# Kernel optimization log

Measured on AMD Instinct MI355X. Metric: run time of the kernel, lower is better.

## Reference

```python
import jax, jax.numpy as jnp
import numpy as np

DIM = 1024
NUM_HEADS = 16
HEAD_DIM = DIM // NUM_HEADS


def setup_inputs() -> dict:
    key = jax.random.key(0)
    ks = jax.random.split(key, 6)
    B, N, C = 2, 2048, DIM
    s = 1.0 / np.sqrt(C)
    return {
        "x": jax.random.normal(ks[0], (B, N, C), dtype=jnp.float32),
        "Wq": jax.random.normal(ks[1], (C, C), dtype=jnp.float32) * s,
        "Wk": jax.random.normal(ks[2], (C, C), dtype=jnp.float32) * s,
        "Wv": jax.random.normal(ks[3], (C, C), dtype=jnp.float32) * s,
        "Wproj": jax.random.normal(ks[4], (C, C), dtype=jnp.float32) * s,
        "bproj": jax.random.normal(ks[5], (C,), dtype=jnp.float32) * 0.01,
    }


def reference(x, Wq, Wk, Wv, Wproj, bproj):
    B, N, C = x.shape
    H, D = NUM_HEADS, HEAD_DIM
    scale = D ** -0.5
    # Linear (torch convention: y = x @ W.T), then split heads -> [B, H, N, D]
    q = (x @ Wq.T).reshape(B, N, H, D).transpose(0, 2, 1, 3)
    k = (x @ Wk.T).reshape(B, N, H, D).transpose(0, 2, 1, 3)
    v = (x @ Wv.T).reshape(B, N, H, D).transpose(0, 2, 1, 3)
    attn = jnp.einsum("bhnd,bhmd->bhnm", q, k) * scale  # [B,H,N,N]
    attn = jax.nn.softmax(attn, axis=-1)
    out = jnp.einsum("bhnm,bhmd->bhnd", attn, v)  # [B,H,N,D]
    out = out.transpose(0, 2, 1, 3).reshape(B, N, C)
    return out @ Wproj.T + bproj
```

## Files before the change

kernel.cpp:

```cpp
#include <hip/hip_runtime.h>
#include <stdint.h>

typedef unsigned short u16;
typedef unsigned int u32;

typedef __bf16 bf16x8 __attribute__((ext_vector_type(8)));
typedef float f32x4 __attribute__((ext_vector_type(4)));

#define LOG2E_SCALE 0.18033688011112042f

static __device__ __forceinline__ u16 f2bf(float f) {
  union { float f; u32 u; } v; v.f = f;
  u32 r = v.u + 0x7fffu + ((v.u >> 16) & 1u);
  return (u16)(r >> 16);
}
static __device__ __forceinline__ u32 pk2(float a, float b) {
  u32 r;
  asm("v_cvt_pk_bf16_f32 %0, %1, %2" : "=v"(r) : "v"(a), "v"(b));
  return r;
}
static __device__ __forceinline__ float fexp2(float x) {
  return __builtin_amdgcn_exp2f(x);
}
static __device__ __forceinline__ float blo(u32 u) {
  union { u32 u; float f; } v; v.u = u << 16; return v.f;
}
static __device__ __forceinline__ float bhi(u32 u) {
  union { u32 u; float f; } v; v.u = u & 0xffff0000u; return v.f;
}

static __device__ __forceinline__ void gl_lds16(const void* g, void* l) {
  __builtin_amdgcn_global_load_lds(
      (const __attribute__((address_space(1))) u32*)g,
      (__attribute__((address_space(3))) u32*)l, 16, 0, 0);
}

__global__ void cast_kernel(const float* __restrict__ x, const float* __restrict__ wq,
                            const float* __restrict__ wk, const float* __restrict__ wv,
                            const float* __restrict__ wp,
                            u16* __restrict__ xb, u16* __restrict__ wqb, u16* __restrict__ wkb,
                            u16* __restrict__ wvb, u16* __restrict__ wpb) {
  const float* src; u16* dst; int n;
  switch (blockIdx.y) {
    case 0: src = x;  dst = xb;  n = 4194304; break;
    case 1: src = wq; dst = wqb; n = 1048576; break;
    case 2: src = wk; dst = wkb; n = 1048576; break;
    case 3: src = wv; dst = wvb; n = 1048576; break;
    default: src = wp; dst = wpb; n = 1048576; break;
  }
  int i = (blockIdx.x * 256 + threadIdx.x) * 8;
  if (i >= n) return;
  float4 a = *(const float4*)(src + i);
  float4 b = *(const float4*)(src + i + 4);
  uint4 o;
  o.x = pk2(a.x, a.y); o.y = pk2(a.z, a.w);
  o.z = pk2(b.x, b.y); o.w = pk2(b.z, b.w);
  *(uint4*)(dst + i) = o;
}

__global__ __launch_bounds__(256, 3) void gemm_qkv(
    const u16* __restrict__ A, const u16* __restrict__ Bq, const u16* __restrict__ Bk,
    const u16* __restrict__ Bv, u16* __restrict__ oQ, u16* __restrict__ oK,
    u16* __restrict__ oVt)
{
  constexpr int K = 1024;
  __shared__ u16 As[128 * 32];
  __shared__ u16 Bs[128 * 32];
  __shared__ float tbuf[4][16 * 68];

  const int tid  = threadIdx.x;
  const int lane = tid & 63;
  const int wave = tid >> 6;
  const int cl   = lane & 15;
  const int g    = lane >> 4;
  const int wm   = (wave >> 1) * 64;
  const int wn   = (wave & 1) * 64;
  const int bm   = blockIdx.y * 128;
  const int bn   = blockIdx.x * 128;
  const int z    = blockIdx.z;
  const u16* B = (z == 0 ? Bq : (z == 1 ? Bk : Bv));

  f32x4 zero4 = {0.f, 0.f, 0.f, 0.f};
  f32x4 acc[4][4];
#pragma unroll
  for (int i = 0; i < 4; i++)
#pragma unroll
    for (int j = 0; j < 4; j++) acc[i][j] = zero4;

  const int srow = tid >> 2;
  const int sch  = (tid & 3) ^ ((srow >> 1) & 3);
  const char* aG = (const char*)(A + (size_t)(bm + srow) * K) + sch * 16;
  const char* bG = (const char*)(B + (size_t)(bn + srow) * K) + sch * 16;
  char* aL = (char*)As + tid * 16;
  char* bL = (char*)Bs + tid * 16;
  const size_t rstep = (size_t)64 * K * 2;

  const int swz = (cl >> 1) & 3;

  for (int k0 = 0; k0 < K; k0 += 32) {
    gl_lds16(aG + k0 * 2, aL);
    gl_lds16(aG + rstep + k0 * 2, aL + 4096);
    gl_lds16(bG + k0 * 2, bL);
    gl_lds16(bG + rstep + k0 * 2, bL + 4096);
    __syncthreads();

    bf16x8 af[4], bf[4];
#pragma unroll
    for (int i = 0; i < 4; i++)
      af[i] = *(const bf16x8*)(As + (wm + i * 16 + cl) * 32 + ((g ^ swz) & 3) * 8);
#pragma unroll
    for (int j = 0; j < 4; j++)
      bf[j] = *(const bf16x8*)(Bs + (wn + j * 16 + cl) * 32 + ((g ^ swz) & 3) * 8);
#pragma unroll
    for (int i = 0; i < 4; i++)
#pragma unroll
      for (int j = 0; j < 4; j++)
        acc[i][j] = __builtin_amdgcn_mfma_f32_16x16x32_bf16(af[i], bf[j], acc[i][j], 0, 0, 0);
    __syncthreads();
  }

  const int rq = g * 4;
  if (z <= 1) {
    u16* o = z ? oK : oQ;
    const float cs = z ? 1.0f : LOG2E_SCALE;
#pragma unroll
    for (int i = 0; i < 4; i++)
#pragma unroll
      for (int j = 0; j < 4; j++)
#pragma unroll
        for (int r = 0; r < 4; r++) {
          int gm = bm + wm + i * 16 + rq + r;
          int gn = bn + wn + j * 16 + cl;
          int b = gm >> 11, ns = gm & 2047;
          int h = gn >> 6,  d  = gn & 63;
          o[(((size_t)(b * 16 + h)) * 2048 + ns) * 64 + d] = f2bf(acc[i][j][r] * cs);
        }
  } else {
    float* tb = tbuf[wave];
#pragma unroll
    for (int j = 0; j < 4; j++) {
      asm volatile("s_waitcnt lgkmcnt(0)" ::: "memory");
#pragma unroll
      for (int i = 0; i < 4; i++)
        *(f32x4*)(tb + cl * 68 + i * 16 + rq) = acc[i][j];
      asm volatile("s_waitcnt lgkmcnt(0)" ::: "memory");
#pragma unroll
      for (int half = 0; half < 2; half++) {
        int dd = lane >> 2, p = (lane & 3) + half * 4;
        f32x4 x0 = *(const f32x4*)(tb + dd * 68 + p * 8);
        f32x4 x1 = *(const f32x4*)(tb + dd * 68 + p * 8 + 4);
        uint4 pkd;
        pkd.x = pk2(x0[0], x0[1]); pkd.y = pk2(x0[2], x0[3]);
        pkd.z = pk2(x1[0], x1[1]); pkd.w = pk2(x1[2], x1[3]);
        int gn = bn + wn + j * 16 + dd;
        int gm = bm + wm + p * 8;
        int b = gm >> 11, nn = gm & 2047;
        int h = gn >> 6,  dl = gn & 63;
        *(uint4*)(oVt + (((size_t)(b * 16 + h)) * 64 + dl) * 2048 + nn) = pkd;
      }
    }
  }
}

__global__ __launch_bounds__(512, 6) void attn_kernel(
    const u16* __restrict__ Q, const u16* __restrict__ Km,
    const u16* __restrict__ Vt, u16* __restrict__ Op, float* __restrict__ lp)
{
  __shared__ u16 ks[2][64 * 64];
  __shared__ u16 vs[2][64 * 64];
  __shared__ u16 ps[128 * 36];

  const int tid  = threadIdx.x;
  const int lane = tid & 63;
  const int W    = tid >> 6;
  const int cl   = lane & 15;
  const int g    = lane >> 4;
  const int bh   = blockIdx.x;
  const int qt   = blockIdx.y;
  const int sp   = blockIdx.z;

  const char* kS = (const char*)Km + (size_t)bh * 2048 * 128 + (size_t)sp * 1024 * 128;
  const char* vS = (const char*)Vt + (size_t)bh * 64 * 4096 + (size_t)sp * 2048;

  const u16* qbase = Q + ((size_t)bh * 2048 + qt * 128 + W * 16) * 64;
  bf16x8 qf[2];
#pragma unroll
  for (int h = 0; h < 2; h++)
    qf[h] = *(const bf16x8*)(qbase + cl * 64 + h * 32 + g * 8);

  auto stage_k = [&](int t) {
    const char* kT = kS + (size_t)t * 8192;
    int kv = tid >> 3, s = tid & 7;
    gl_lds16(kT + kv * 128 + (((s ^ kv) & 7) * 16), (char*)ks[t & 1] + tid * 16);
  };
  auto stage_v = [&](int t) {
    const char* vT = vS + (size_t)t * 128;
    int d = tid >> 3, s = tid & 7;
    gl_lds16(vT + (size_t)d * 4096 + (((s ^ d) & 7) * 16), (char*)vs[t & 1] + tid * 16);
  };

  stage_k(0);
  stage_v(0);

  f32x4 zero4 = {0.f, 0.f, 0.f, 0.f};
  f32x4 o_acc[4];
#pragma unroll
  for (int j = 0; j < 4; j++) o_acc[j] = zero4;
  float li = 0.f;

  for (int t = 0; t < 16; ++t) {
    __syncthreads();
    if (t < 15) { stage_k(t + 1); stage_v(t + 1); }

    const u16* kb = ks[t & 1];
    const u16* vb = vs[t & 1];

    f32x4 st[4];
#pragma unroll
    for (int j = 0; j < 4; j++) st[j] = zero4;
#pragma unroll
    for (int h = 0; h < 2; h++) {
#pragma unroll
      for (int j = 0; j < 4; j++) {
        bf16x8 kf = *(const bf16x8*)(kb + (j * 16 + cl) * 64 + (((h * 4 + g) ^ (cl & 7)) & 7) * 8);
        st[j] = __builtin_amdgcn_mfma_f32_16x16x32_bf16(kf, qf[h], st[j], 0, 0, 0);
      }
    }

#pragma unroll
    for (int j = 0; j < 4; j++)
#pragma unroll
      for (int r = 0; r < 4; r++) {
        float p = fexp2(st[j][r]);
        st[j][r] = p;
        li += p;
      }

    char* prow = (char*)ps + (W * 16 + cl) * 72;
#pragma unroll
    for (int h32 = 0; h32 < 2; h32++) {
#pragma unroll
      for (int jj = 0; jj < 2; jj++) {
        int j = h32 * 2 + jj;
        uint2 w;
        w.x = pk2(st[j][0], st[j][1]);
        w.y = pk2(st[j][2], st[j][3]);
        *(uint2*)(prow + jj * 32 + g * 8) = w;
      }
      bf16x8 pf, vf[4];
      union { bf16x8 v; uint2 u[2]; } pu;
      pu.u[0] = *(const uint2*)(prow + g * 16);
      pu.u[1] = *(const uint2*)(prow + g * 16 + 8);
      pf = pu.v;
#pragma unroll
      for (int j = 0; j < 4; j++)
        vf[j] = *(const bf16x8*)(vb + (j * 16 + cl) * 64 + (((h32 * 4 + g) ^ (cl & 7)) & 7) * 8);
#pragma unroll
      for (int j = 0; j < 4; j++)
        o_acc[j] = __builtin_amdgcn_mfma_f32_16x16x32_bf16(pf, vf[j], o_acc[j], 0, 0, 0);
    }
  }

  li += __shfl_xor(li, 16, 64);
  li += __shfl_xor(li, 32, 64);
  const int b = bh >> 4, hh = bh & 15;
  u16* Os = Op + (size_t)sp * 4194304;
  float* ls = lp + sp * 65536;
  if (g == 0) ls[bh * 2048 + qt * 128 + W * 16 + cl] = li;
#pragma unroll
  for (int r = 0; r < 4; r++) {
    int row = qt * 128 + W * 16 + g * 4 + r;
    u16* orow = Os + ((size_t)b * 2048 + row) * 1024 + hh * 64;
#pragma unroll
    for (int j = 0; j < 4; j++)
      orow[j * 16 + cl] = f2bf(o_acc[j][r]);
  }
}

__global__ void reduce_o(const u16* __restrict__ Op, const float* __restrict__ lp,
                         u16* __restrict__ Ow) {
  int t = blockIdx.x * 256 + threadIdx.x;
  int idx = t * 8;
  int b   = idx >> 21;
  int rem = idx & 2097151;
  int row = rem >> 10;
  int h   = (rem & 1023) >> 6;
  int lidx = (b * 16 + h) * 2048 + row;
  float inv = 1.0f / (lp[lidx] + lp[65536 + lidx]);
  uint4 a = *(const uint4*)(Op + idx);
  uint4 c = *(const uint4*)(Op + 4194304 + idx);
  uint4 o;
  o.x = pk2((blo(a.x) + blo(c.x)) * inv, (bhi(a.x) + bhi(c.x)) * inv);
  o.y = pk2((blo(a.y) + blo(c.y)) * inv, (bhi(a.y) + bhi(c.y)) * inv);
  o.z = pk2((blo(a.z) + blo(c.z)) * inv, (bhi(a.z) + bhi(c.z)) * inv);
  o.w = pk2((blo(a.w) + blo(c.w)) * inv, (bhi(a.w) + bhi(c.w)) * inv);
  *(uint4*)(Ow + idx) = o;
}

__global__ __launch_bounds__(256, 4) void proj_gemm(
    const u16* __restrict__ A, const u16* __restrict__ B,
    float* __restrict__ out, const float* __restrict__ bias)
{
  constexpr int K = 1024;
  __shared__ u16 As[64 * 32];
  __shared__ u16 Bs[128 * 32];

  const int tid  = threadIdx.x;
  const int lane = tid & 63;
  const int wave = tid >> 6;
  const int cl   = lane & 15;
  const int g    = lane >> 4;
  const int wm   = (wave >> 1) * 32;
  const int wn   = (wave & 1) * 64;
  const int bm   = blockIdx.y * 64;
  const int bn   = blockIdx.x * 128;

  f32x4 zero4 = {0.f, 0.f, 0.f, 0.f};
  f32x4 acc[2][4];
#pragma unroll
  for (int i = 0; i < 2; i++)
#pragma unroll
    for (int j = 0; j < 4; j++) acc[i][j] = zero4;

  const int srow = tid >> 2;
  const int sch  = (tid & 3) ^ ((srow >> 1) & 3);
  const char* aG = (const char*)(A + (size_t)(bm + srow) * K) + sch * 16;
  const char* bG = (const char*)(B + (size_t)(bn + srow) * K) + sch * 16;
  char* aL = (char*)As + tid * 16;
  char* bL = (char*)Bs + tid * 16;
  const size_t rstep = (size_t)64 * K * 2;

  const int swz = (cl >> 1) & 3;

  for (int k0 = 0; k0 < K; k0 += 32) {
    gl_lds16(aG + k0 * 2, aL);
    gl_lds16(bG + k0 * 2, bL);
    gl_lds16(bG + rstep + k0 * 2, bL + 4096);
    __syncthreads();

    bf16x8 af[2], bf[4];
#pragma unroll
    for (int i = 0; i < 2; i++)
      af[i] = *(const bf16x8*)(As + (wm + i * 16 + cl) * 32 + ((g ^ swz) & 3) * 8);
#pragma unroll
    for (int j = 0; j < 4; j++)
      bf[j] = *(const bf16x8*)(Bs + (wn + j * 16 + cl) * 32 + ((g ^ swz) & 3) * 8);
#pragma unroll
    for (int i = 0; i < 2; i++)
#pragma unroll
      for (int j = 0; j < 4; j++)
        acc[i][j] = __builtin_amdgcn_mfma_f32_16x16x32_bf16(af[i], bf[j], acc[i][j], 0, 0, 0);
    __syncthreads();
  }

  const int rq = g * 4;
#pragma unroll
  for (int i = 0; i < 2; i++)
#pragma unroll
    for (int j = 0; j < 4; j++)
#pragma unroll
      for (int r = 0; r < 4; r++) {
        int gm = bm + wm + i * 16 + rq + r;
        int gn = bn + wn + j * 16 + cl;
        out[(size_t)gm * 1024 + gn] = acc[i][j][r] + bias[gn];
      }
}

extern "C" void kernel_launch(void* const* d_in, const int* in_sizes, int n_in,
                              void* d_out, int out_size, void* d_ws, size_t ws_size,
                              hipStream_t stream) {
  const float* x     = (const float*)d_in[0];
  const float* Wq    = (const float*)d_in[1];
  const float* Wk    = (const float*)d_in[2];
  const float* Wv    = (const float*)d_in[3];
  const float* Wp    = (const float*)d_in[4];
  const float* bproj = (const float*)d_in[5];

  u16* ws  = (u16*)d_ws;
  u16* xb  = ws;
  u16* wqb = xb + 4194304;
  u16* wkb = wqb + 1048576;
  u16* wvb = wkb + 1048576;
  u16* wpb = wvb + 1048576;
  u16* Qw  = wpb + 1048576;
  u16* Kw  = Qw + 4194304;
  u16* Vw  = Kw + 4194304;
  u16* Ow  = Vw + 4194304;
  u16* Opart = Ow + 4194304;
  float* lpart = (float*)(Opart + 8388608);
  (void)in_sizes; (void)n_in; (void)out_size; (void)ws_size;

  cast_kernel<<<dim3(2048, 5), 256, 0, stream>>>(x, Wq, Wk, Wv, Wp, xb, wqb, wkb, wvb, wpb);
  gemm_qkv<<<dim3(8, 32, 3), 256, 0, stream>>>(xb, wqb, wkb, wvb, Qw, Kw, Vw);
  attn_kernel<<<dim3(32, 16, 2), 512, 0, stream>>>(Qw, Kw, Vw, Opart, lpart);
  reduce_o<<<dim3(2048), 256, 0, stream>>>(Opart, lpart, Ow);
  proj_gemm<<<dim3(8, 64), 256, 0, stream>>>(Ow, wpb, (float*)d_out, bproj);
}
```

Measured before the change: 183.9 us.

## Double K-tile depth in QKV and projection GEMMs and compute row sums via MFMA

Both GEMM kernels now stage a 64-wide K slab per iteration with an 8-way XOR swizzle, which halves the number of barrier pairs and loop iterations. The QKV kernel reuses the A tile's shared memory as its transpose buffer, so the larger tiles do not increase LDS usage beyond the old footprint. In attention, the softmax denominator is accumulated by an extra MFMA against a ones vector instead of scalar adds and cross-lane shuffles. The cost is one extra MFMA per PV step, and the row sum is now taken over bf16-rounded probabilities rather than fp32 ones.

Result: faster. 178.9 us (-2.7%).

```diff
diff --git a/kernel.cpp b/kernel.cpp
--- a/kernel.cpp
+++ b/kernel.cpp
@@ -64,9 +64,8 @@
     u16* __restrict__ oVt)
 {
   constexpr int K = 1024;
-  __shared__ u16 As[128 * 32];
-  __shared__ u16 Bs[128 * 32];
-  __shared__ float tbuf[4][16 * 68];
+  __shared__ u16 As[128 * 64];
+  __shared__ u16 Bs[128 * 64];
 
   const int tid  = threadIdx.x;
   const int lane = tid & 63;
@@ -87,35 +86,37 @@
 #pragma unroll
     for (int j = 0; j < 4; j++) acc[i][j] = zero4;
 
-  const int srow = tid >> 2;
-  const int sch  = (tid & 3) ^ ((srow >> 1) & 3);
-  const char* aG = (const char*)(A + (size_t)(bm + srow) * K) + sch * 16;
-  const char* bG = (const char*)(B + (size_t)(bn + srow) * K) + sch * 16;
+  const int srow = tid >> 3;
+  const int sch  = (tid & 7) ^ (srow & 7);
+  const char* aG = (const char*)(A + (size_t)(bm + srow) * K + sch * 8);
+  const char* bG = (const char*)(B + (size_t)(bn + srow) * K + sch * 8);
   char* aL = (char*)As + tid * 16;
   char* bL = (char*)Bs + tid * 16;
-  const size_t rstep = (size_t)64 * K * 2;
-
-  const int swz = (cl >> 1) & 3;
-
-  for (int k0 = 0; k0 < K; k0 += 32) {
-    gl_lds16(aG + k0 * 2, aL);
-    gl_lds16(aG + rstep + k0 * 2, aL + 4096);
-    gl_lds16(bG + k0 * 2, bL);
-    gl_lds16(bG + rstep + k0 * 2, bL + 4096);
+  const size_t rstep = (size_t)32 * K * 2;
+
+  for (int k0 = 0; k0 < K; k0 += 64) {
+#pragma unroll
+    for (int r = 0; r < 4; r++) {
+      gl_lds16(aG + r * rstep + k0 * 2, aL + r * 4096);
+      gl_lds16(bG + r * rstep + k0 * 2, bL + r * 4096);
+    }
     __syncthreads();
 
-    bf16x8 af[4], bf[4];
-#pragma unroll
-    for (int i = 0; i < 4; i++)
-      af[i] = *(const bf16x8*)(As + (wm + i * 16 + cl) * 32 + ((g ^ swz) & 3) * 8);
-#pragma unroll
-    for (int j = 0; j < 4; j++)
-      bf[j] = *(const bf16x8*)(Bs + (wn + j * 16 + cl) * 32 + ((g ^ swz) & 3) * 8);
-#pragma unroll
-    for (int i = 0; i < 4; i++)
+#pragma unroll
+    for (int kk = 0; kk < 2; kk++) {
+      bf16x8 af[4], bf[4];
+#pragma unroll
+      for (int i = 0; i < 4; i++)
+        af[i] = *(const bf16x8*)(As + (wm + i * 16 + cl) * 64 + (((kk * 4 + g) ^ (cl & 7)) * 8));
 #pragma unroll
       for (int j = 0; j < 4; j++)
-        acc[i][j] = __builtin_amdgcn_mfma_f32_16x16x32_bf16(af[i], bf[j], acc[i][j], 0, 0, 0);
+        bf[j] = *(const bf16x8*)(Bs + (wn + j * 16 + cl) * 64 + (((kk * 4 + g) ^ (cl & 7)) * 8));
+#pragma unroll
+      for (int i = 0; i < 4; i++)
+#pragma unroll
+        for (int j = 0; j < 4; j++)
+          acc[i][j] = __builtin_amdgcn_mfma_f32_16x16x32_bf16(af[i], bf[j], acc[i][j], 0, 0, 0);
+    }
     __syncthreads();
   }
 
@@ -136,7 +137,7 @@
           o[(((size_t)(b * 16 + h)) * 2048 + ns) * 64 + d] = f2bf(acc[i][j][r] * cs);
         }
   } else {
-    float* tb = tbuf[wave];
+    float* tb = (float*)As + wave * (16 * 68);
 #pragma unroll
     for (int j = 0; j < 4; j++) {
       asm volatile("s_waitcnt lgkmcnt(0)" ::: "memory");
@@ -188,6 +189,11 @@
   for (int h = 0; h < 2; h++)
     qf[h] = *(const bf16x8*)(qbase + cl * 64 + h * 32 + g * 8);
 
+  union { bf16x8 v; u32 u[4]; } onesu;
+#pragma unroll
+  for (int k = 0; k < 4; k++) onesu.u[k] = 0x3f803f80u;
+  const bf16x8 onesf = onesu.v;
+
   auto stage_k = [&](int t) {
     const char* kT = kS + (size_t)t * 8192;
     int kv = tid >> 3, s = tid & 7;
@@ -206,7 +212,7 @@
   f32x4 o_acc[4];
 #pragma unroll
   for (int j = 0; j < 4; j++) o_acc[j] = zero4;
-  float li = 0.f;
+  f32x4 l_acc = zero4;
 
   for (int t = 0; t < 16; ++t) {
     __syncthreads();
@@ -230,11 +236,8 @@
 #pragma unroll
     for (int j = 0; j < 4; j++)
 #pragma unroll
-      for (int r = 0; r < 4; r++) {
-        float p = fexp2(st[j][r]);
-        st[j][r] = p;
-        li += p;
-      }
+      for (int r = 0; r < 4; r++)
+        st[j][r] = fexp2(st[j][r]);
 
     char* prow = (char*)ps + (W * 16 + cl) * 72;
 #pragma unroll
@@ -258,15 +261,18 @@
 #pragma unroll
       for (int j = 0; j < 4; j++)
         o_acc[j] = __builtin_amdgcn_mfma_f32_16x16x32_bf16(pf, vf[j], o_acc[j], 0, 0, 0);
-    }
-  }
-
-  li += __shfl_xor(li, 16, 64);
-  li += __shfl_xor(li, 32, 64);
+      l_acc = __builtin_amdgcn_mfma_f32_16x16x32_bf16(pf, onesf, l_acc, 0, 0, 0);
+    }
+  }
+
   const int b = bh >> 4, hh = bh & 15;
   u16* Os = Op + (size_t)sp * 4194304;
   float* ls = lp + sp * 65536;
-  if (g == 0) ls[bh * 2048 + qt * 128 + W * 16 + cl] = li;
+  if (cl == 0) {
+#pragma unroll
+    for (int r = 0; r < 4; r++)
+      ls[bh * 2048 + qt * 128 + W * 16 + g * 4 + r] = l_acc[r];
+  }
 #pragma unroll
   for (int r = 0; r < 4; r++) {
     int row = qt * 128 + W * 16 + g * 4 + r;
@@ -302,8 +308,8 @@
     float* __restrict__ out, const float* __restrict__ bias)
 {
   constexpr int K = 1024;
-  __shared__ u16 As[64 * 32];
-  __shared__ u16 Bs[128 * 32];
+  __shared__ u16 As[64 * 64];
+  __shared__ u16 Bs[128 * 64];
 
   const int tid  = threadIdx.x;
   const int lane = tid & 63;
@@ -322,34 +328,38 @@
 #pragma unroll
     for (int j = 0; j < 4; j++) acc[i][j] = zero4;
 
-  const int srow = tid >> 2;
-  const int sch  = (tid & 3) ^ ((srow >> 1) & 3);
-  const char* aG = (const char*)(A + (size_t)(bm + srow) * K) + sch * 16;
-  const char* bG = (const char*)(B + (size_t)(bn + srow) * K) + sch * 16;
+  const int srow = tid >> 3;
+  const int sch  = (tid & 7) ^ (srow & 7);
+  const char* aG = (const char*)(A + (size_t)(bm + srow) * K + sch * 8);
+  const char* bG = (const char*)(B + (size_t)(bn + srow) * K + sch * 8);
   char* aL = (char*)As + tid * 16;
   char* bL = (char*)Bs + tid * 16;
-  const size_t rstep = (size_t)64 * K * 2;
-
-  const int swz = (cl >> 1) & 3;
-
-  for (int k0 = 0; k0 < K; k0 += 32) {
-    gl_lds16(aG + k0 * 2, aL);
-    gl_lds16(bG + k0 * 2, bL);
-    gl_lds16(bG + rstep + k0 * 2, bL + 4096);
+  const size_t rstep = (size_t)32 * K * 2;
+
+  for (int k0 = 0; k0 < K; k0 += 64) {
+#pragma unroll
+    for (int r = 0; r < 2; r++)
+      gl_lds16(aG + r * rstep + k0 * 2, aL + r * 4096);
+#pragma unroll
+    for (int r = 0; r < 4; r++)
+      gl_lds16(bG + r * rstep + k0 * 2, bL + r * 4096);
     __syncthreads();
 
-    bf16x8 af[2], bf[4];
-#pragma unroll
-    for (int i = 0; i < 2; i++)
-      af[i] = *(const bf16x8*)(As + (wm + i * 16 + cl) * 32 + ((g ^ swz) & 3) * 8);
-#pragma unroll
-    for (int j = 0; j < 4; j++)
-      bf[j] = *(const bf16x8*)(Bs + (wn + j * 16 + cl) * 32 + ((g ^ swz) & 3) * 8);
-#pragma unroll
-    for (int i = 0; i < 2; i++)
+#pragma unroll
+    for (int kk = 0; kk < 2; kk++) {
+      bf16x8 af[2], bf[4];
+#pragma unroll
+      for (int i = 0; i < 2; i++)
+        af[i] = *(const bf16x8*)(As + (wm + i * 16 + cl) * 64 + (((kk * 4 + g) ^ (cl & 7)) * 8));
 #pragma unroll
       for (int j = 0; j < 4; j++)
-        acc[i][j] = __builtin_amdgcn_mfma_f32_16x16x32_bf16(af[i], bf[j], acc[i][j], 0, 0, 0);
+        bf[j] = *(const bf16x8*)(Bs + (wn + j * 16 + cl) * 64 + (((kk * 4 + g) ^ (cl & 7)) * 8));
+#pragma unroll
+      for (int i = 0; i < 2; i++)
+#pragma unroll
+        for (int j = 0; j < 4; j++)
+          acc[i][j] = __builtin_amdgcn_mfma_f32_16x16x32_bf16(af[i], bf[j], acc[i][j], 0, 0, 0);
+    }
     __syncthreads();
   }
 
```
